# Kernel optimization log

Hardware: AMD Instinct MI355X
Metric: run time of the kernel (lower is better)

Reference implementation:

```python
import jax, jax.numpy as jnp
import numpy as np

N_QUBITS = 8
N_LAYERS = 2
BATCH = 8192


def _rx(theta):
    # theta: scalar or (batch,) -> (...,2,2) complex64
    c = jnp.cos(theta / 2) + 0j
    s = jnp.sin(theta / 2)
    off = -1j * s
    return jnp.stack([jnp.stack([c, off], -1), jnp.stack([off, c], -1)], -2)


def _ry(theta):
    c = jnp.cos(theta / 2) + 0j
    s = jnp.sin(theta / 2) + 0j
    return jnp.stack([jnp.stack([c, -s], -1), jnp.stack([s, c], -1)], -2)


def _rz(theta):
    e = jnp.exp(-1j * theta / 2)
    z = jnp.zeros_like(e)
    return jnp.stack([jnp.stack([e, z], -1), jnp.stack([z, jnp.conj(e)], -1)], -2)


def _apply_shared(state, gate, wire):
    # state: (batch, 2,...,2); gate: (2,2) shared across batch
    ax = 1 + wire
    st = jnp.moveaxis(state, ax, -1)
    st = jnp.einsum('...i,ji->...j', st, gate)
    return jnp.moveaxis(st, -1, ax)


def _apply_batched(state, gate, wire):
    # gate: (batch, 2, 2), one gate per batch element (data-encoding RX)
    ax = 1 + wire
    st = jnp.moveaxis(state, ax, -1)
    shp = st.shape
    st = st.reshape(shp[0], -1, 2)
    st = jnp.einsum('bki,bji->bkj', st, gate)
    return jnp.moveaxis(st.reshape(shp), -1, ax)


def _cnot(state, ctrl, tgt):
    axc, axt = 1 + ctrl, 1 + tgt
    st = jnp.moveaxis(state, (axc, axt), (-2, -1))
    st = jnp.stack([st[..., 0, :], st[..., 1, ::-1]], axis=-2)
    return jnp.moveaxis(st, (-2, -1), (axc, axt))


def _circuit(x, params):
    batch = x.shape[0]
    dim = 2 ** N_QUBITS
    state = jnp.zeros((batch, dim), dtype=jnp.complex64).at[:, 0].set(1.0)
    state = state.reshape((batch,) + (2,) * N_QUBITS)
    # data encoding
    for i in range(N_QUBITS):
        state = _apply_batched(state, _rx(x[:, i]), i)
    # variational layers
    for l in range(N_LAYERS):
        for i in range(N_QUBITS):
            state = _apply_shared(state, _ry(params[l, i, 0]), i)
            state = _apply_shared(state, _rz(params[l, i, 1]), i)
            if i < N_QUBITS - 1:
                state = _cnot(state, i, i + 1)
        for i in range(N_QUBITS):
            state = _apply_shared(state, _rx(params[l, i, 2]), i)
    # <Z_i> = P(bit_i=0) - P(bit_i=1)
    probs = state.real ** 2 + state.imag ** 2  # (batch, 2,...,2)
    outs = []
    for i in range(N_QUBITS):
        p = jnp.moveaxis(probs, 1 + i, 1).reshape(batch, 2, -1).sum(-1)
        outs.append(p[:, 0] - p[:, 1])
    return jnp.stack(outs, axis=-1)  # (batch, n_qubits)


def setup_inputs() -> dict:
    key = jax.random.key(0)
    kx, kp = jax.random.split(key)
    x = jax.random.normal(kx, (BATCH, N_QUBITS), dtype=jnp.float32)
    params = jax.random.normal(kp, (N_LAYERS, N_QUBITS, 3), dtype=jnp.float32)
    return {"x": x, "params": params}


def reference(x, params):
    return _circuit(x, params)
```

## Files before the change

kernel.cpp:

```cpp
#include <hip/hip_runtime.h>

#define DEV __device__ __forceinline__

typedef unsigned u32;
typedef u32 u32x2 __attribute__((ext_vector_type(2)));
typedef _Float16 f16;
typedef f16   f16x8 __attribute__((ext_vector_type(8)));
typedef float f32x4 __attribute__((ext_vector_type(4)));

template<int CTRL>
DEV int dpp_full(int src) {
    return __builtin_amdgcn_update_dpp(src, src, CTRL, 0xF, 0xF, false);
}
template<int CTRL, int RM, int BM>
DEV int dpp_masked(int old, int src) {
    return __builtin_amdgcn_update_dpp(old, src, CTRL, RM, BM, false);
}

template<int B>
DEV float lshfl(float x, bool px) {
    int xi = __float_as_int(x);
    if constexpr (B == 0) {
        return __int_as_float(dpp_full<0xB1>(xi));
    } else if constexpr (B == 1) {
        return __int_as_float(dpp_full<0x4E>(xi));
    } else if constexpr (B == 2) {
        return __int_as_float(__builtin_amdgcn_ds_swizzle(xi, 0x101F));
    } else if constexpr (B == 3) {
        return __int_as_float(dpp_full<0x128>(xi));
    } else if constexpr (B == 4) {
        return __int_as_float(__builtin_amdgcn_ds_swizzle(xi, 0x401F));
    } else {
        u32x2 r = __builtin_amdgcn_permlane32_swap((u32)xi, (u32)xi, false, false);
        return __int_as_float((int)(px ? r.x : r.y));
    }
}

DEV bool probe32(int lane) {
    u32 p = (u32)((lane >> 5) & 1);
    u32x2 r = __builtin_amdgcn_permlane32_swap(p, p, false, false);
    return r.x == (p ^ 1u);
}

DEV void rx_pair(float& r0, float& i0, float& r1, float& i1, float c, float s) {
    float nr0 = fmaf(c, r0,  s * i1);
    float ni0 = fmaf(c, i0, -s * r1);
    float nr1 = fmaf(c, r1,  s * i0);
    float ni1 = fmaf(c, i1, -s * r0);
    r0 = nr0; i0 = ni0; r1 = nr1; i1 = ni1;
}
DEV void ry_pair(float& r0, float& i0, float& r1, float& i1, float c, float s) {
    float nr0 = fmaf(c, r0, -s * r1);
    float ni0 = fmaf(c, i0, -s * i1);
    float nr1 = fmaf(c, r1,  s * r0);
    float ni1 = fmaf(c, i1,  s * i0);
    r0 = nr0; i0 = ni0; r1 = nr1; i1 = ni1;
}
DEV void rz_amp(float& r, float& i, float c, float ss) {
    float nr = fmaf(c, r, -ss * i);
    float ni = fmaf(c, i,  ss * r);
    r = nr; i = ni;
}

template<int B>
DEV void apply_rx(float (&re)[4], float (&im)[4], int lane, bool px, float c, float s) {
    if constexpr (B == 7) {
        rx_pair(re[0], im[0], re[2], im[2], c, s);
        rx_pair(re[1], im[1], re[3], im[3], c, s);
    } else if constexpr (B == 6) {
        rx_pair(re[0], im[0], re[1], im[1], c, s);
        rx_pair(re[2], im[2], re[3], im[3], c, s);
    } else {
#pragma unroll
        for (int k = 0; k < 4; ++k) {
            float pr = lshfl<B>(re[k], px);
            float pi = lshfl<B>(im[k], px);
            re[k] = fmaf(c, re[k],  s * pi);
            im[k] = fmaf(c, im[k], -s * pr);
        }
    }
}
template<int B>
DEV void apply_ry(float (&re)[4], float (&im)[4], int lane, bool px, float c, float s) {
    if constexpr (B == 7) {
        ry_pair(re[0], im[0], re[2], im[2], c, s);
        ry_pair(re[1], im[1], re[3], im[3], c, s);
    } else if constexpr (B == 6) {
        ry_pair(re[0], im[0], re[1], im[1], c, s);
        ry_pair(re[2], im[2], re[3], im[3], c, s);
    } else {
        float ssel = ((lane >> B) & 1) ? s : -s;
#pragma unroll
        for (int k = 0; k < 4; ++k) {
            float pr = lshfl<B>(re[k], px);
            float pi = lshfl<B>(im[k], px);
            re[k] = fmaf(c, re[k], ssel * pr);
            im[k] = fmaf(c, im[k], ssel * pi);
        }
    }
}
template<int B>
DEV void apply_rz(float (&re)[4], float (&im)[4], int lane, float c, float s) {
    if constexpr (B == 7) {
        rz_amp(re[0], im[0], c, -s); rz_amp(re[1], im[1], c, -s);
        rz_amp(re[2], im[2], c,  s); rz_amp(re[3], im[3], c,  s);
    } else if constexpr (B == 6) {
        rz_amp(re[0], im[0], c, -s); rz_amp(re[1], im[1], c,  s);
        rz_amp(re[2], im[2], c, -s); rz_amp(re[3], im[3], c,  s);
    } else {
        float ss = ((lane >> B) & 1) ? s : -s;
#pragma unroll
        for (int k = 0; k < 4; ++k) rz_amp(re[k], im[k], c, ss);
    }
}
template<int BC, int BT>
DEV void apply_cnot(float (&re)[4], float (&im)[4], int lane, bool px) {
    if constexpr (BC == 7 && BT == 6) {
        float tr = re[2], ti = im[2];
        re[2] = re[3]; im[2] = im[3];
        re[3] = tr;    im[3] = ti;
    } else if constexpr (BC == 6) {
        re[1] = lshfl<5>(re[1], px); im[1] = lshfl<5>(im[1], px);
        re[3] = lshfl<5>(re[3], px); im[3] = lshfl<5>(im[3], px);
    } else if constexpr (BC == 5 && BT == 4) {
        bool ctrl = (lane >> 5) & 1;
#pragma unroll
        for (int k = 0; k < 4; ++k) {
            float pr = lshfl<4>(re[k], px);
            float pi = lshfl<4>(im[k], px);
            re[k] = ctrl ? pr : re[k];
            im[k] = ctrl ? pi : im[k];
        }
    } else if constexpr (BC == 4 && BT == 3) {
#pragma unroll
        for (int k = 0; k < 4; ++k) {
            int r = __float_as_int(re[k]), i = __float_as_int(im[k]);
            re[k] = __int_as_float(dpp_masked<0x128, 0xA, 0xF>(r, r));
            im[k] = __int_as_float(dpp_masked<0x128, 0xA, 0xF>(i, i));
        }
    } else if constexpr (BC == 3 && BT == 2) {
#pragma unroll
        for (int k = 0; k < 4; ++k) {
            int r = __float_as_int(re[k]), i = __float_as_int(im[k]);
            int tr = dpp_full<0x1B>(r), ti = dpp_full<0x1B>(i);
            re[k] = __int_as_float(dpp_masked<0x141, 0xF, 0xC>(r, tr));
            im[k] = __int_as_float(dpp_masked<0x141, 0xF, 0xC>(i, ti));
        }
    } else if constexpr (BC == 2 && BT == 1) {
#pragma unroll
        for (int k = 0; k < 4; ++k) {
            int r = __float_as_int(re[k]), i = __float_as_int(im[k]);
            re[k] = __int_as_float(dpp_masked<0x4E, 0xF, 0xA>(r, r));
            im[k] = __int_as_float(dpp_masked<0x4E, 0xF, 0xA>(i, i));
        }
    } else {
#pragma unroll
        for (int k = 0; k < 4; ++k) {
            re[k] = __int_as_float(dpp_full<0xB4>(__float_as_int(re[k])));
            im[k] = __int_as_float(dpp_full<0xB4>(__float_as_int(im[k])));
        }
    }
}


__global__ __launch_bounds__(512) void qa_genU(
    const float* __restrict__ params, f16* __restrict__ Bg, f16* __restrict__ Bh)
{
    __shared__ float gs[96];
    __shared__ f16 Lg[8][256];
    __shared__ f16 Lh[8][256];

    int tid  = threadIdx.x;
    int w    = tid >> 6, lane = tid & 63;
    int j    = blockIdx.x * 8 + w;
    bool px  = probe32(lane);

    if (tid < 48) {
        float th = params[tid] * 0.5f;
        gs[2 * tid]     = __cosf(th);
        gs[2 * tid + 1] = __sinf(th);
    }
    __syncthreads();

    float re[4], im[4];
#pragma unroll
    for (int k = 0; k < 4; ++k) {
        re[k] = ((j >> 6) == k && (j & 63) == lane) ? 1.f : 0.f;
        im[k] = 0.f;
    }

#define VQ(l, i) { const int jj = (l) * 24 + (i) * 3;                       \
                   apply_ry<7 - (i)>(re, im, lane, px, gs[2*jj],   gs[2*jj+1]); \
                   apply_rz<7 - (i)>(re, im, lane,     gs[2*jj+2], gs[2*jj+3]); }
#define CN(i)    apply_cnot<7 - (i), 6 - (i)>(re, im, lane, px);
#define RXQ(l,i) { const int jj = (l) * 24 + (i) * 3 + 2;                   \
                   apply_rx<7 - (i)>(re, im, lane, px, gs[2*jj], gs[2*jj+1]); }
#define LAYER(l) \
    VQ(l,0) CN(0) VQ(l,1) CN(1) VQ(l,2) CN(2) VQ(l,3) CN(3) \
    VQ(l,4) CN(4) VQ(l,5) CN(5) VQ(l,6) CN(6) VQ(l,7)       \
    RXQ(l,0) RXQ(l,1) RXQ(l,2) RXQ(l,3) RXQ(l,4) RXQ(l,5) RXQ(l,6) RXQ(l,7)

    LAYER(0)
    LAYER(1)
#undef LAYER
#undef RXQ
#undef CN
#undef VQ

    int sel = __popc((u32)j) & 3;
#pragma unroll
    for (int k = 0; k < 4; ++k) {
        int idx = k * 64 + lane;
        float g, h;
        if      (sel == 0) { g =  re[k]; h =  im[k]; }
        else if (sel == 1) { g =  im[k]; h = -re[k]; }
        else if (sel == 2) { g = -re[k]; h = -im[k]; }
        else               { g = -im[k]; h =  re[k]; }
        Lg[w][idx] = (f16)g;
        Lh[w][idx] = (f16)h;
    }
    __syncthreads();

    {
        int idx  = tid & 255;
        bool ish = tid >= 256;
        const f16* src = ish ? &Lh[0][0] : &Lg[0][0];
        f16x8 v;
#pragma unroll
        for (int wv = 0; wv < 8; ++wv) v[wv] = src[wv * 256 + idx];
        f16* dst = ish ? Bh : Bg;
        int kb = blockIdx.x >> 2, joff = (blockIdx.x & 3) * 8;
        *reinterpret_cast<f16x8*>(&dst[(kb * 256 + idx) * 32 + joff]) = v;
    }
}


__global__ __launch_bounds__(512, 2) void qa_gemm(
    const float* __restrict__ x,
    const f16* __restrict__ Bg, const f16* __restrict__ Bh,
    float* __restrict__ out, int batch)
{
    __shared__ __align__(16) f16 Ap[32 * 256];
    __shared__ float zb[4][32][8];

    int tid  = threadIdx.x;
    int w    = tid >> 6, lane = tid & 63;
    int rg   = w >> 2,   cg   = w & 3;
    int b0   = blockIdx.x * 32;
    if (b0 >= batch) return;

#pragma unroll
    for (int e = 0; e < 4; ++e) {
        int rl = w * 4 + e;
        const float* xb = x + (b0 + rl) * 8;
        float4 xlo = *(const float4*)xb;
        float4 xhi = *(const float4*)(xb + 4);
        float c_[8], s_[8];
        __sincosf(xlo.x * 0.5f, &s_[0], &c_[0]);
        __sincosf(xlo.y * 0.5f, &s_[1], &c_[1]);
        __sincosf(xlo.z * 0.5f, &s_[2], &c_[2]);
        __sincosf(xlo.w * 0.5f, &s_[3], &c_[3]);
        __sincosf(xhi.x * 0.5f, &s_[4], &c_[4]);
        __sincosf(xhi.y * 0.5f, &s_[5], &c_[5]);
        __sincosf(xhi.z * 0.5f, &s_[6], &c_[6]);
        __sincosf(xhi.w * 0.5f, &s_[7], &c_[7]);

        float m6;
        m6  = ((lane >> 5) & 1) ? s_[2] : c_[2];
        m6 *= ((lane >> 4) & 1) ? s_[3] : c_[3];
        m6 *= ((lane >> 3) & 1) ? s_[4] : c_[4];
        m6 *= ((lane >> 2) & 1) ? s_[5] : c_[5];
        m6 *= ((lane >> 1) & 1) ? s_[6] : c_[6];
        m6 *= ( lane       & 1) ? s_[7] : c_[7];
        float kf[4] = { c_[0] * c_[1], c_[0] * s_[1], s_[0] * c_[1], s_[0] * s_[1] };
        int sw = (rl & 7) << 3;
#pragma unroll
        for (int k = 0; k < 4; ++k) {
            int j  = k * 64 + lane;
            int hi = rl * 256 + (j ^ sw);
            Ap[hi] = (f16)(m6 * kf[k]);
        }
    }
    __syncthreads();

    f32x4 accR[4], accI[4];
#pragma unroll
    for (int t = 0; t < 4; ++t) { accR[t] = (f32x4)0.f; accI[t] = (f32x4)0.f; }

    int colbase = cg * 64 + (lane & 15);
    int arow    = rg * 16 + (lane & 15);
    int kg      = lane >> 4;
    const f16x8* B8g = reinterpret_cast<const f16x8*>(Bg);
    const f16x8* B8h = reinterpret_cast<const f16x8*>(Bh);

#pragma unroll
    for (int kb = 0; kb < 8; ++kb) {
        int afi = arow * 32 + ((kb * 4 + kg) ^ (arow & 7));
        f16x8 ap = *reinterpret_cast<const f16x8*>(&Ap[afi * 8]);
#pragma unroll
        for (int t = 0; t < 4; ++t) {
            int idx = colbase + t * 16;
            int bo  = (kb * 256 + idx) * 4 + kg;
            f16x8 bg = B8g[bo];
            f16x8 bh = B8h[bo];
            accR[t] = __builtin_amdgcn_mfma_f32_16x16x32_f16(ap, bg, accR[t], 0, 0, 0);
            accI[t] = __builtin_amdgcn_mfma_f32_16x16x32_f16(ap, bh, accI[t], 0, 0, 0);
        }
    }

    float z[4][8];
#pragma unroll
    for (int r = 0; r < 4; ++r)
#pragma unroll
        for (int q = 0; q < 8; ++q) z[r][q] = 0.f;

#pragma unroll
    for (int t = 0; t < 4; ++t) {
        int idx = colbase + t * 16;
#pragma unroll
        for (int r = 0; r < 4; ++r) {
            float cr = accR[t][r], ci = accI[t][r];
            float p = fmaf(cr, cr, ci * ci);
#pragma unroll
            for (int q = 0; q < 8; ++q)
                z[r][q] += ((idx >> (7 - q)) & 1) ? -p : p;
        }
    }

#pragma unroll
    for (int r = 0; r < 4; ++r)
#pragma unroll
        for (int q = 0; q < 8; ++q) {
            z[r][q] += lshfl<0>(z[r][q], false);
            z[r][q] += lshfl<1>(z[r][q], false);
            z[r][q] += lshfl<2>(z[r][q], false);
            z[r][q] += lshfl<3>(z[r][q], false);
        }

    if ((lane & 15) < 8) {
        int q = lane & 7;
#pragma unroll
        for (int r = 0; r < 4; ++r)
            zb[cg][rg * 16 + (lane >> 4) * 4 + r][q] = z[r][q];
    }
    __syncthreads();

    if (tid < 256) {
        int row = tid >> 3, q = tid & 7;
        float v = zb[0][row][q] + zb[1][row][q] + zb[2][row][q] + zb[3][row][q];
        out[(b0 + row) * 8 + q] = v;
    }
}

extern "C" void kernel_launch(void* const* d_in, const int* in_sizes, int n_in,
                              void* d_out, int out_size, void* d_ws, size_t ws_size,
                              hipStream_t stream) {
    const float* x      = (const float*)d_in[0];
    const float* params = (const float*)d_in[1];
    float* out = (float*)d_out;

    f16* Bg = (f16*)d_ws;
    f16* Bh = Bg + 65536;

    int batch = in_sizes[0] / 8;

    qa_genU<<<32, 512, 0, stream>>>(params, Bg, Bh);

    int blocks = (batch + 31) / 32;
    qa_gemm<<<blocks, 512, 0, stream>>>(x, Bg, Bh, out, batch);
}
```

Measured before the change: 25.32 us.

## Halve rows per block in qa_gemm and use butterfly reduction for Z expectations

```diff
diff --git a/kernel.cpp b/kernel.cpp
--- a/kernel.cpp
+++ b/kernel.cpp
@@ -235,24 +235,24 @@
 }
 
 
-__global__ __launch_bounds__(512, 2) void qa_gemm(
+__global__ __launch_bounds__(512, 4) void qa_gemm(
     const float* __restrict__ x,
     const f16* __restrict__ Bg, const f16* __restrict__ Bh,
     float* __restrict__ out, int batch)
 {
-    __shared__ __align__(16) f16 Ap[32 * 256];
-    __shared__ float zb[4][32][8];
+    __shared__ __align__(16) f16 Ap[16 * 256];
+    __shared__ float zb[8][16][8];
 
     int tid  = threadIdx.x;
     int w    = tid >> 6, lane = tid & 63;
-    int rg   = w >> 2,   cg   = w & 3;
-    int b0   = blockIdx.x * 32;
+    int b0   = blockIdx.x * 16;
     if (b0 >= batch) return;
 
 #pragma unroll
-    for (int e = 0; e < 4; ++e) {
-        int rl = w * 4 + e;
-        const float* xb = x + (b0 + rl) * 8;
+    for (int e = 0; e < 2; ++e) {
+        int rl = w * 2 + e;
+        int bb = b0 + rl; if (bb >= batch) bb = batch - 1;
+        const float* xb = x + bb * 8;
         float4 xlo = *(const float4*)xb;
         float4 xhi = *(const float4*)(xb + 4);
         float c_[8], s_[8];
@@ -283,12 +283,13 @@
     }
     __syncthreads();
 
-    f32x4 accR[4], accI[4];
-#pragma unroll
-    for (int t = 0; t < 4; ++t) { accR[t] = (f32x4)0.f; accI[t] = (f32x4)0.f; }
-
-    int colbase = cg * 64 + (lane & 15);
-    int arow    = rg * 16 + (lane & 15);
+    f32x4 accR[2], accI[2];
+#pragma unroll
+    for (int t = 0; t < 2; ++t) { accR[t] = (f32x4)0.f; accI[t] = (f32x4)0.f; }
+
+    int L       = lane & 15;
+    int colbase = w * 32 + L;
+    int arow    = L;
     int kg      = lane >> 4;
     const f16x8* B8g = reinterpret_cast<const f16x8*>(Bg);
     const f16x8* B8h = reinterpret_cast<const f16x8*>(Bh);
@@ -298,7 +299,7 @@
         int afi = arow * 32 + ((kb * 4 + kg) ^ (arow & 7));
         f16x8 ap = *reinterpret_cast<const f16x8*>(&Ap[afi * 8]);
 #pragma unroll
-        for (int t = 0; t < 4; ++t) {
+        for (int t = 0; t < 2; ++t) {
             int idx = colbase + t * 16;
             int bo  = (kb * 256 + idx) * 4 + kg;
             f16x8 bg = B8g[bo];
@@ -308,47 +309,46 @@
         }
     }
 
-    float z[4][8];
-#pragma unroll
-    for (int r = 0; r < 4; ++r)
-#pragma unroll
-        for (int q = 0; q < 8; ++q) z[r][q] = 0.f;
-
-#pragma unroll
-    for (int t = 0; t < 4; ++t) {
-        int idx = colbase + t * 16;
-#pragma unroll
-        for (int r = 0; r < 4; ++r) {
-            float cr = accR[t][r], ci = accI[t][r];
-            float p = fmaf(cr, cr, ci * ci);
-#pragma unroll
-            for (int q = 0; q < 8; ++q)
-                z[r][q] += ((idx >> (7 - q)) & 1) ? -p : p;
-        }
-    }
-
-#pragma unroll
-    for (int r = 0; r < 4; ++r)
-#pragma unroll
-        for (int q = 0; q < 8; ++q) {
-            z[r][q] += lshfl<0>(z[r][q], false);
-            z[r][q] += lshfl<1>(z[r][q], false);
-            z[r][q] += lshfl<2>(z[r][q], false);
-            z[r][q] += lshfl<3>(z[r][q], false);
-        }
-
-    if ((lane & 15) < 8) {
-        int q = lane & 7;
-#pragma unroll
-        for (int r = 0; r < 4; ++r)
-            zb[cg][rg * 16 + (lane >> 4) * 4 + r][q] = z[r][q];
+    bool wr = (L < 8);
+#pragma unroll
+    for (int r = 0; r < 4; ++r) {
+        float p0 = fmaf(accR[0][r], accR[0][r], accI[0][r] * accI[0][r]);
+        float p1 = fmaf(accR[1][r], accR[1][r], accI[1][r] * accI[1][r]);
+        float S = p0 + p1;
+        float T = p0 - p1;
+
+        float P;
+        P = lshfl<0>(S, false); float w0d = S - P; S += P;
+        P = lshfl<1>(S, false); float w1d = S - P; S += P;
+        P = lshfl<2>(S, false); float w2d = S - P; S += P;
+        P = lshfl<3>(S, false); float w3d = S - P; S += P;
+        w0d += lshfl<1>(w0d, false); w0d += lshfl<2>(w0d, false); w0d += lshfl<3>(w0d, false);
+        w1d += lshfl<2>(w1d, false); w1d += lshfl<3>(w1d, false);
+        w2d += lshfl<3>(w2d, false);
+
+        T += lshfl<0>(T, false); T += lshfl<1>(T, false);
+        T += lshfl<2>(T, false); T += lshfl<3>(T, false);
+
+        if (wr) {
+            float val = (L == 0) ? ((w & 4) ? -S : S)
+                      : (L == 1) ? ((w & 2) ? -S : S)
+                      : (L == 2) ? ((w & 1) ? -S : S)
+                      : (L == 3) ? T
+                      : (L == 4) ? w3d
+                      : (L == 5) ? -w2d
+                      : (L == 6) ? -w1d
+                      :            -w0d;
+            zb[w][(lane >> 4) * 4 + r][L] = val;
+        }
     }
     __syncthreads();
 
-    if (tid < 256) {
+    if (tid < 128) {
         int row = tid >> 3, q = tid & 7;
-        float v = zb[0][row][q] + zb[1][row][q] + zb[2][row][q] + zb[3][row][q];
-        out[(b0 + row) * 8 + q] = v;
+        float v = 0.f;
+#pragma unroll
+        for (int g = 0; g < 8; ++g) v += zb[g][row][q];
+        if (b0 + row < batch) out[(b0 + row) * 8 + q] = v;
     }
 }
 
@@ -366,6 +366,6 @@
 
     qa_genU<<<32, 512, 0, stream>>>(params, Bg, Bh);
 
-    int blocks = (batch + 31) / 32;
+    int blocks = (batch + 15) / 16;
     qa_gemm<<<blocks, 512, 0, stream>>>(x, Bg, Bh, out, batch);
 }
```

Measured after the change: 22.23 us. 1.14x faster.
